# Optimization experiments

Measured on AMD Instinct MI355X. Metric: run time of the kernel, lower is better.

## Reference

```python
import jax, jax.numpy as jnp
import numpy as np

B, NQ, NK = 4, 2048, 2048
DQ = DK = DV = 256
H = 8
HD = DV // H
EPS = 1e-5


def _ln(x, g, b):
    m = jnp.mean(x, axis=-1, keepdims=True)
    v = jnp.mean(jnp.square(x - m), axis=-1, keepdims=True)
    return (x - m) * jax.lax.rsqrt(v + EPS) * g + b


def setup_inputs() -> dict:
    key = jax.random.key(0)
    ks = jax.random.split(key, 12)
    s = 0.02
    return {
        "Q": jax.random.normal(ks[0], (B, NQ, DQ), jnp.float32),
        "K": jax.random.normal(ks[1], (B, NK, DK), jnp.float32),
        "Wq": jax.random.normal(ks[2], (DV, DQ), jnp.float32) * s,
        "bq": jnp.zeros((DV,), jnp.float32),
        "Wk": jax.random.normal(ks[3], (DV, DK), jnp.float32) * s,
        "bk": jnp.zeros((DV,), jnp.float32),
        "Wv": jax.random.normal(ks[4], (DV, DK), jnp.float32) * s,
        "bv": jnp.zeros((DV,), jnp.float32),
        "Wo": jax.random.normal(ks[5], (DV, DV), jnp.float32) * s,
        "bo": jnp.zeros((DV,), jnp.float32),
        "g0": jnp.ones((DV,), jnp.float32),
        "b0": jnp.zeros((DV,), jnp.float32),
        "g1": jnp.ones((DV,), jnp.float32),
        "b1": jnp.zeros((DV,), jnp.float32),
    }


def reference(Q, K, Wq, bq, Wk, bk, Wv, bv, Wo, bo, g0, b0, g1, b1):
    Qp = Q @ Wq.T + bq            # [B,NQ,DV]
    Kp = K @ Wk.T + bk            # [B,NK,DV]
    Vp = K @ Wv.T + bv            # [B,NK,DV]
    # split(head_dim, dim=2) + cat(dim=0) == reshape heads from contiguous channel chunks
    qh = Qp.reshape(B, NQ, H, HD)
    kh = Kp.reshape(B, NK, H, HD)
    vh = Vp.reshape(B, NK, H, HD)
    scores = jnp.einsum("bqhd,bkhd->bhqk", qh, kh) / jnp.sqrt(jnp.float32(HD))
    attn = jax.nn.softmax(scores, axis=-1)          # [B,H,NQ,NK]
    o = jnp.einsum("bhqk,bkhd->bqhd", attn, vh).reshape(B, NQ, DV)
    o = _ln(o, g0, b0)
    out = o + jax.nn.relu(o @ Wo.T + bo)
    out = _ln(out, g1, b1)
    return out
```

## Files before the change

kernel.cpp:

```cpp
#include <hip/hip_runtime.h>
#include <hip/hip_bf16.h>
#include <math.h>

#define DV 256
#define NH 8
#define NB 4
#define NQ 2048
#define NKK 2048

typedef __attribute__((ext_vector_type(8))) short s8v;
typedef __attribute__((ext_vector_type(16))) float fx16;

typedef const __attribute__((address_space(1))) char g1c;
typedef __attribute__((address_space(3))) char l3c;

__device__ __forceinline__ void gl_lds16(const void* g, void* l) {
    __builtin_amdgcn_global_load_lds((g1c*)g, (l3c*)l, 16, 0, 0);
}
__device__ __forceinline__ unsigned cvtpk_bf16(float lo, float hi) {
    unsigned r;
    asm("v_cvt_pk_bf16_f32 %0, %1, %2" : "=v"(r) : "v"(lo), "v"(hi));
    return r;
}
__device__ __forceinline__ ushort f2bf(float x) {
    unsigned u = __builtin_bit_cast(unsigned, x);
    return (ushort)((u + 0x7fffu + ((u >> 16) & 1u)) >> 16);
}
__device__ __forceinline__ float bf2f(ushort h) {
    return __builtin_bit_cast(float, (unsigned)h << 16);
}

__global__ __launch_bounds__(256) void prep_w_k(
    const float* __restrict__ Wq, const float* __restrict__ Wk,
    const float* __restrict__ Wv, const float* __restrict__ Wo,
    ushort* __restrict__ Wf)
{
    const int j = blockIdx.x * 256 + threadIdx.x;
    const int w = j >> 13, c = j & 8191;
    const int bn = c >> 11, s = (c >> 8) & 7, cc = c & 255;
    const int colblk = cc >> 7, ks = (cc >> 6) & 1, g5w = (cc >> 5) & 1, l31w = cc & 31;
    const int col = bn * 64 + colblk * 32 + l31w;
    const int k = s * 32 + ks * 16 + g5w * 8;
    const float* Wsrc = (w == 0) ? Wq : (w == 1) ? Wk : (w == 2) ? Wv : Wo;
    const float* src = Wsrc + (size_t)col * 256 + k;
    float4 a = *(const float4*)src;
    float4 b = *(const float4*)(src + 4);
    uint4 pk;
    pk.x = cvtpk_bf16(a.x, a.y); pk.y = cvtpk_bf16(a.z, a.w);
    pk.z = cvtpk_bf16(b.x, b.y); pk.w = cvtpk_bf16(b.z, b.w);
    *(uint4*)(Wf + (size_t)j * 8) = pk;
}

__global__ __launch_bounds__(256) void gemm_qkv_k(
    const float* __restrict__ Qf, const float* __restrict__ Kf,
    const ushort* __restrict__ Wf,
    const float* __restrict__ bq, const float* __restrict__ bk, const float* __restrict__ bv,
    ushort* __restrict__ Qb, ushort* __restrict__ Kb, ushort* __restrict__ Vt)
{
    __shared__ __align__(16) char lds[2][20480];
    const int t = threadIdx.x, lane = t & 63, wv = t >> 6;
    const int l31 = lane & 31, g5 = lane >> 5;
    const int bm = blockIdx.x, bn = blockIdx.y;
    const int z = blockIdx.z;
    const float* Af = (z == 0) ? Qf : Kf;
    const ushort* WF = Wf + (size_t)z * 65536;
    const float* bias = (z == 0) ? bq : (z == 1) ? bk : bv;

    int arow[4], aoff[4];
#pragma unroll
    for (int k = 0; k < 4; ++k) {
        const int q = k * 256 + t, c = q >> 1, p = q & 1;
        arow[k] = bm * 128 + (c >> 7) * 32 + (c & 31);
        aoff[k] = ((c >> 6) & 1) * 16 + ((c >> 5) & 1) * 8 + p * 4;
    }
    const ushort* wsrc = WF + (size_t)(bn * 8) * 2048 + t * 8;

#pragma unroll
    for (int k = 0; k < 4; ++k)
        gl_lds16(Af + (size_t)arow[k] * 256 + aoff[k],
                 &lds[0][k * 4096 + wv * 1024 + lane * 16]);
    gl_lds16(wsrc, &lds[0][16384 + wv * 1024 + lane * 16]);
    __syncthreads();

    fx16 acc0 = {}, acc1 = {};
    for (int s = 0; s < 8; ++s) {
        const int buf = s & 1;
        if (s + 1 < 8) {
#pragma unroll
            for (int k = 0; k < 4; ++k)
                gl_lds16(Af + (size_t)arow[k] * 256 + (s + 1) * 32 + aoff[k],
                         &lds[buf ^ 1][k * 4096 + wv * 1024 + lane * 16]);
            gl_lds16(wsrc + (s + 1) * 2048, &lds[buf ^ 1][16384 + wv * 1024 + lane * 16]);
        }
        const char* Al = lds[buf];
        const char* Wl = lds[buf] + 16384;
        float4 fa0 = *(const float4*)(Al + (wv * 2 + 0) * 2048 + lane * 32);
        float4 fb0 = *(const float4*)(Al + (wv * 2 + 0) * 2048 + lane * 32 + 16);
        float4 fa1 = *(const float4*)(Al + (wv * 2 + 1) * 2048 + lane * 32);
        float4 fb1 = *(const float4*)(Al + (wv * 2 + 1) * 2048 + lane * 32 + 16);
        union { unsigned u[4]; s8v v; } A0, A1;
        A0.u[0] = cvtpk_bf16(fa0.x, fa0.y); A0.u[1] = cvtpk_bf16(fa0.z, fa0.w);
        A0.u[2] = cvtpk_bf16(fb0.x, fb0.y); A0.u[3] = cvtpk_bf16(fb0.z, fb0.w);
        A1.u[0] = cvtpk_bf16(fa1.x, fa1.y); A1.u[1] = cvtpk_bf16(fa1.z, fa1.w);
        A1.u[2] = cvtpk_bf16(fb1.x, fb1.y); A1.u[3] = cvtpk_bf16(fb1.z, fb1.w);
        s8v b00 = *(const s8v*)(Wl + 0 * 1024 + lane * 16);
        s8v b01 = *(const s8v*)(Wl + 1 * 1024 + lane * 16);
        s8v b10 = *(const s8v*)(Wl + 2 * 1024 + lane * 16);
        s8v b11 = *(const s8v*)(Wl + 3 * 1024 + lane * 16);
        __builtin_amdgcn_s_setprio(1);
        acc0 = __builtin_amdgcn_mfma_f32_32x32x16_bf16(A0.v, b00, acc0, 0, 0, 0);
        acc0 = __builtin_amdgcn_mfma_f32_32x32x16_bf16(A1.v, b01, acc0, 0, 0, 0);
        acc1 = __builtin_amdgcn_mfma_f32_32x32x16_bf16(A0.v, b10, acc1, 0, 0, 0);
        acc1 = __builtin_amdgcn_mfma_f32_32x32x16_bf16(A1.v, b11, acc1, 0, 0, 0);
        __builtin_amdgcn_s_setprio(0);
        __syncthreads();
    }

    const int row_b = bm * 128 + wv * 32;
    const float CE = 0.17677669529663687f * 1.4426950408889634f;
    const float bs0 = bias[bn * 64 + l31];
    const float bs1 = bias[bn * 64 + 32 + l31];
    if (z == 0) {
#pragma unroll
        for (int r = 0; r < 16; ++r) {
            const int row_g = row_b + (r & 3) + 8 * (r >> 2) + 4 * g5;
            Qb[(size_t)row_g * 256 + bn * 64 + l31]      = f2bf((acc0[r] + bs0) * CE);
            Qb[(size_t)row_g * 256 + bn * 64 + 32 + l31] = f2bf((acc1[r] + bs1) * CE);
        }
    } else if (z == 1) {
#pragma unroll
        for (int r = 0; r < 16; ++r) {
            const int row_g = row_b + (r & 3) + 8 * (r >> 2) + 4 * g5;
            Kb[(size_t)row_g * 256 + bn * 64 + l31]      = f2bf(acc0[r] + bs0);
            Kb[(size_t)row_g * 256 + bn * 64 + 32 + l31] = f2bf(acc1[r] + bs1);
        }
    } else {
#pragma unroll
        for (int r = 0; r < 16; ++r) {
            const int row_g = row_b + (r & 3) + 8 * (r >> 2) + 4 * g5;
            const int bb = row_g >> 11, n = row_g & 2047;
            Vt[((size_t)(bb * 8 + bn * 2 + 0) * 32 + l31) * 2048 + n] = f2bf(acc0[r] + bs0);
            Vt[((size_t)(bb * 8 + bn * 2 + 1) * 32 + l31) * 2048 + n] = f2bf(acc1[r] + bs1);
        }
    }
}

__global__ __launch_bounds__(256) void flash_mfma_k(
    const ushort* __restrict__ Qb, const ushort* __restrict__ Kb,
    const ushort* __restrict__ Vt, ushort* __restrict__ Osb, float* __restrict__ L)
{
    __shared__ __align__(16) char lds[2][8192];
    const int t = threadIdx.x;
    const int lane = t & 63, wv = t >> 6;
    const int l31 = lane & 31, g5 = lane >> 5;
    const int qt = blockIdx.x, h = blockIdx.y;
    const int b = blockIdx.z >> 1, sp = blockIdx.z & 1;

    s8v qf0, qf1;
    {
        const ushort* qp = Qb + (((size_t)b * NQ + qt * 128 + wv * 32 + l31) << 8) + h * 32 + g5 * 8;
        qf0 = *(const s8v*)(qp);
        qf1 = *(const s8v*)(qp + 16);
    }
    s8v ones;
#pragma unroll
    for (int j = 0; j < 8; ++j) ones[j] = (short)0x3F80;

    const ushort* ksrc = Kb + (((size_t)b * NKK + sp * 1024 + ((t >> 7) * 32 + (t & 31))) << 8)
                            + h * 32 + ((t >> 6) & 1) * 16 + ((t >> 5) & 1) * 8;
    const ushort* vsrc = Vt + (((size_t)(b * NH + h) * 32 + (t & 31)) << 11) + sp * 1024
                            + (t >> 6) * 16 + ((t >> 5) & 1) * 8;

    fx16 O0 = {}, lsum = {};

    gl_lds16(ksrc, &lds[0][wv * 1024]);
    gl_lds16(vsrc, &lds[0][4096 + wv * 1024]);
    __syncthreads();

    for (int kt = 0; kt < 16; ++kt) {
        const int buf = kt & 1;
        if (kt + 1 < 16) {
            gl_lds16(ksrc + (size_t)(kt + 1) * 64 * DV, &lds[buf ^ 1][wv * 1024]);
            gl_lds16(vsrc + (kt + 1) * 64, &lds[buf ^ 1][4096 + wv * 1024]);
        }
        const char* Kl = lds[buf];
        const char* Vl = lds[buf] + 4096;
        s8v kf00 = *(const s8v*)(Kl + 0 * 1024 + lane * 16);
        s8v kf01 = *(const s8v*)(Kl + 1 * 1024 + lane * 16);
        s8v kf10 = *(const s8v*)(Kl + 2 * 1024 + lane * 16);
        s8v kf11 = *(const s8v*)(Kl + 3 * 1024 + lane * 16);
        s8v vfa[4];
        vfa[0] = *(const s8v*)(Vl + 0 * 1024 + lane * 16);
        vfa[1] = *(const s8v*)(Vl + 1 * 1024 + lane * 16);
        vfa[2] = *(const s8v*)(Vl + 2 * 1024 + lane * 16);
        vfa[3] = *(const s8v*)(Vl + 3 * 1024 + lane * 16);

        fx16 z = {};
        __builtin_amdgcn_s_setprio(1);
        fx16 Sa = __builtin_amdgcn_mfma_f32_32x32x16_bf16(kf00, qf0, z, 0, 0, 0);
        Sa = __builtin_amdgcn_mfma_f32_32x32x16_bf16(kf01, qf1, Sa, 0, 0, 0);
        fx16 Sb = __builtin_amdgcn_mfma_f32_32x32x16_bf16(kf10, qf0, z, 0, 0, 0);
        Sb = __builtin_amdgcn_mfma_f32_32x32x16_bf16(kf11, qf1, Sb, 0, 0, 0);
        __builtin_amdgcn_s_setprio(0);

        float p[32];
#pragma unroll
        for (int i = 0; i < 16; ++i) {
            p[i]      = __builtin_amdgcn_exp2f(Sa[i]);
            p[16 + i] = __builtin_amdgcn_exp2f(Sb[i]);
        }

        __builtin_amdgcn_s_setprio(1);
#pragma unroll
        for (int kt2 = 0; kt2 < 4; ++kt2) {
            const int pb = 8 * kt2;
            auto ra = __builtin_amdgcn_permlane32_swap(
                cvtpk_bf16(p[pb + 0], p[pb + 1]), cvtpk_bf16(p[pb + 4], p[pb + 5]), false, false);
            auto rb = __builtin_amdgcn_permlane32_swap(
                cvtpk_bf16(p[pb + 2], p[pb + 3]), cvtpk_bf16(p[pb + 6], p[pb + 7]), false, false);
            union { unsigned u[4]; s8v v; } pf;
            pf.u[0] = ra[0]; pf.u[1] = rb[0]; pf.u[2] = ra[1]; pf.u[3] = rb[1];
            O0   = __builtin_amdgcn_mfma_f32_32x32x16_bf16(vfa[kt2], pf.v, O0, 0, 0, 0);
            lsum = __builtin_amdgcn_mfma_f32_32x32x16_bf16(ones,    pf.v, lsum, 0, 0, 0);
        }
        __builtin_amdgcn_s_setprio(0);
        __syncthreads();
    }

    {
        const int qrow = qt * 128 + wv * 32 + l31;
        ushort* dst0 = Osb + (size_t)sp * (8192 * 256)
                     + (((size_t)b * NQ + qrow) << 8) + h * 32 + g5 * 4;
#pragma unroll
        for (int rr = 0; rr < 4; ++rr) {
            uint2 w;
            w.x = cvtpk_bf16(O0[4 * rr + 0], O0[4 * rr + 1]);
            w.y = cvtpk_bf16(O0[4 * rr + 2], O0[4 * rr + 3]);
            *(uint2*)(dst0 + 8 * rr) = w;
        }
        if (g5 == 0)
            L[(((size_t)sp * NB + b) * NH + h) * NQ + qrow] = lsum[0];
    }
}

__global__ __launch_bounds__(256) void comb_ln_k(
    const ushort* __restrict__ Osb, const float* __restrict__ L,
    const float* __restrict__ g, const float* __restrict__ bb,
    ushort* __restrict__ Yb)
{
    const int t = threadIdx.x, lane = t & 63, w = t >> 6;
    const int row = blockIdx.x * 4 + w;
    const int b = row >> 11, q = row & 2047;
    const int h = lane >> 3;
    const size_t lbase = (((size_t)b * NH + h) * NQ + q);
    const size_t LS = (size_t)NB * NH * NQ;
    const float inv = 1.f / (L[lbase] + L[LS + lbase]);
    const size_t SZS = (size_t)8192 * 256;
    const size_t off = (size_t)row * 256 + lane * 4;
    const ushort4 x0 = *(const ushort4*)(Osb + off);
    const ushort4 x1 = *(const ushort4*)(Osb + SZS + off);
    float4 x;
    x.x = (bf2f(x0.x) + bf2f(x1.x)) * inv;
    x.y = (bf2f(x0.y) + bf2f(x1.y)) * inv;
    x.z = (bf2f(x0.z) + bf2f(x1.z)) * inv;
    x.w = (bf2f(x0.w) + bf2f(x1.w)) * inv;
    float s  = (x.x + x.y) + (x.z + x.w);
    float sq = fmaf(x.x, x.x, fmaf(x.y, x.y, fmaf(x.z, x.z, x.w * x.w)));
    for (int off2 = 32; off2; off2 >>= 1) {
        s  += __shfl_xor(s, off2);
        sq += __shfl_xor(sq, off2);
    }
    const float mean = s * (1.f / 256.f);
    const float var  = sq * (1.f / 256.f) - mean * mean;
    const float ri   = rsqrtf(var + 1e-5f);
    const float4 gv = *(const float4*)(g + lane * 4);
    const float4 bv = *(const float4*)(bb + lane * 4);
    uint2 p;
    p.x = cvtpk_bf16((x.x - mean) * ri * gv.x + bv.x, (x.y - mean) * ri * gv.y + bv.y);
    p.y = cvtpk_bf16((x.z - mean) * ri * gv.z + bv.z, (x.w - mean) * ri * gv.w + bv.w);
    *(uint2*)(Yb + (size_t)row * 256 + lane * 4) = p;
}

__global__ __launch_bounds__(256) void gemm_ln_k(
    const ushort* __restrict__ Ain, const ushort* __restrict__ Wfo,
    const float* __restrict__ bo, const float* __restrict__ g1,
    const float* __restrict__ b1, float* __restrict__ out)
{
    __shared__ __align__(16) char alds[32768];
    __shared__ __align__(16) char wlds[2][16384];
    __shared__ float red[4][64][2];
    __shared__ float par[64][2];
    const int t = threadIdx.x, lane = t & 63, wv = t >> 6;
    const int l31 = lane & 31, g5 = lane >> 5;
    const int row0 = blockIdx.x * 64;

#pragma unroll
    for (int it = 0; it < 8; ++it) {
        const int id = it * 256 + t;
        const int s = id >> 8, rem = id & 255, kc = rem >> 6, row = rem & 63;
        gl_lds16(Ain + (size_t)(row0 + row) * 256 + s * 32 + (kc >> 1) * 16 + (kc & 1) * 8,
                 &alds[id * 16]);
    }
#pragma unroll
    for (int it = 0; it < 4; ++it) {
        const int id = it * 256 + t;
        gl_lds16(Wfo + ((size_t)(id >> 8) * 2048 + (id & 255)) * 8, &wlds[0][id * 16]);
    }
    __syncthreads();

    fx16 acc[2][2] = {};
    for (int s = 0; s < 8; ++s) {
        const int buf = s & 1;
        if (s + 1 < 8) {
#pragma unroll
            for (int it = 0; it < 4; ++it) {
                const int id = it * 256 + t;
                gl_lds16(Wfo + ((size_t)(id >> 8) * 2048 + (s + 1) * 256 + (id & 255)) * 8,
                         &wlds[buf ^ 1][id * 16]);
            }
        }
        s8v a[2][2], bf[2][2];
#pragma unroll
        for (int rb = 0; rb < 2; ++rb)
#pragma unroll
            for (int ks = 0; ks < 2; ++ks)
                a[rb][ks] = *(const s8v*)(alds + ((s * 4 + ks * 2 + g5) * 64 + rb * 32 + l31) * 16);
#pragma unroll
        for (int ks = 0; ks < 2; ++ks)
#pragma unroll
            for (int ch = 0; ch < 2; ++ch)
                bf[ks][ch] = *(const s8v*)(wlds[buf] + (wv * 256 + ch * 128 + ks * 64 + g5 * 32 + l31) * 16);
        __builtin_amdgcn_s_setprio(1);
#pragma unroll
        for (int rb = 0; rb < 2; ++rb)
#pragma unroll
            for (int ch = 0; ch < 2; ++ch) {
                acc[rb][ch] = __builtin_amdgcn_mfma_f32_32x32x16_bf16(a[rb][0], bf[0][ch], acc[rb][ch], 0, 0, 0);
                acc[rb][ch] = __builtin_amdgcn_mfma_f32_32x32x16_bf16(a[rb][1], bf[1][ch], acc[rb][ch], 0, 0, 0);
            }
        __builtin_amdgcn_s_setprio(0);
        __syncthreads();
    }

    const int cg0 = wv * 64 + l31, cg1 = cg0 + 32;
    const float bo0 = bo[cg0], bo1 = bo[cg1];
    const int s0 = cg0 >> 5, kk0 = cg0 & 31;
    const int s1 = cg1 >> 5, kk1 = cg1 & 31;
    const int coff0 = (s0 * 4 + ((kk0 >> 4) << 1) + ((kk0 >> 3) & 1)) * 64;
    const int coff1 = (s1 * 4 + ((kk1 >> 4) << 1) + ((kk1 >> 3) & 1)) * 64;
    float x[2][2][16];
#pragma unroll
    for (int rb = 0; rb < 2; ++rb) {
#pragma unroll
        for (int r = 0; r < 16; ++r) {
            const int row = rb * 32 + (r & 3) + 8 * (r >> 2) + 4 * g5;
            const ushort h0v = *(const ushort*)(alds + ((coff0 + row) << 4) + (kk0 & 7) * 2);
            const ushort h1v = *(const ushort*)(alds + ((coff1 + row) << 4) + (kk1 & 7) * 2);
            const float x0 = bf2f(h0v) + fmaxf(acc[rb][0][r] + bo0, 0.f);
            const float x1 = bf2f(h1v) + fmaxf(acc[rb][1][r] + bo1, 0.f);
            x[rb][0][r] = x0; x[rb][1][r] = x1;
            float sv = x0 + x1;
            float sq = fmaf(x0, x0, x1 * x1);
#pragma unroll
            for (int off = 1; off < 32; off <<= 1) {
                sv += __shfl_xor(sv, off);
                sq += __shfl_xor(sq, off);
            }
            if (l31 == 0) { red[wv][row][0] = sv; red[wv][row][1] = sq; }
        }
    }
    __syncthreads();
    if (t < 64) {
        const float sv = (red[0][t][0] + red[1][t][0]) + (red[2][t][0] + red[3][t][0]);
        const float sq = (red[0][t][1] + red[1][t][1]) + (red[2][t][1] + red[3][t][1]);
        const float mean = sv * (1.f / 256.f);
        const float var  = sq * (1.f / 256.f) - mean * mean;
        par[t][0] = mean;
        par[t][1] = rsqrtf(var + 1e-5f);
    }
    __syncthreads();
    const float g1a = g1[cg0], g1b = g1[cg1];
    const float b1a = b1[cg0], b1b = b1[cg1];
#pragma unroll
    for (int rb = 0; rb < 2; ++rb) {
#pragma unroll
        for (int r = 0; r < 16; ++r) {
            const int row = rb * 32 + (r & 3) + 8 * (r >> 2) + 4 * g5;
            const float mean = par[row][0], ri = par[row][1];
            out[(size_t)(row0 + row) * 256 + cg0] = (x[rb][0][r] - mean) * ri * g1a + b1a;
            out[(size_t)(row0 + row) * 256 + cg1] = (x[rb][1][r] - mean) * ri * g1b + b1b;
        }
    }
}

extern "C" void kernel_launch(void* const* d_in, const int* in_sizes, int n_in,
                              void* d_out, int out_size, void* d_ws, size_t ws_size,
                              hipStream_t stream) {
    const float* Q  = (const float*)d_in[0];
    const float* K  = (const float*)d_in[1];
    const float* Wq = (const float*)d_in[2];
    const float* bq = (const float*)d_in[3];
    const float* Wk = (const float*)d_in[4];
    const float* bk = (const float*)d_in[5];
    const float* Wv = (const float*)d_in[6];
    const float* bv = (const float*)d_in[7];
    const float* Wo = (const float*)d_in[8];
    const float* bo = (const float*)d_in[9];
    const float* g0 = (const float*)d_in[10];
    const float* b0 = (const float*)d_in[11];
    const float* g1 = (const float*)d_in[12];
    const float* b1 = (const float*)d_in[13];
    float* out = (float*)d_out;

    char* wsb = (char*)d_ws;
    const size_t MB = 1u << 20;
    ushort* Wf  = (ushort*)(wsb + 12 * MB);
    ushort* Qb  = (ushort*)(wsb + 0 * MB);
    ushort* Kb  = (ushort*)(wsb + 4 * MB);
    ushort* Vt  = (ushort*)(wsb + 8 * MB);
    ushort* Osb = (ushort*)(wsb + 13 * MB);
    float*  L   = (float*)(wsb + 21 * MB);
    ushort* h0b = (ushort*)(wsb + 8 * MB);

    prep_w_k<<<128, 256, 0, stream>>>(Wq, Wk, Wv, Wo, Wf);
    gemm_qkv_k<<<dim3(64, 4, 3), 256, 0, stream>>>(Q, K, Wf, bq, bk, bv, Qb, Kb, Vt);
    flash_mfma_k<<<dim3(16, 8, 8), 256, 0, stream>>>(Qb, Kb, Vt, Osb, L);
    comb_ln_k<<<2048, 256, 0, stream>>>(Osb, L, g0, b0, h0b);
    gemm_ln_k<<<128, 256, 0, stream>>>(h0b, Wf + 3 * 65536, bo, g1, b1, out);
}
```

Measured before the change: 78.44 us.

## Fuse split-KV combine and first LayerNorm into output-projection GEMM kernel

Merges the combine+LayerNorm kernel into the Wo GEMM + residual + LayerNorm kernel. Each block now combines the two split partial outputs, normalizes them, and writes bf16 rows straight into LDS in the MFMA A-operand layout, so the intermediate h0 buffer never goes through global memory and one launch disappears. Block rows drop from 64 to 32, giving 256 blocks instead of 128 for better CU coverage. In exchange, each block reloads all of Wo and does half as much MFMA work per weight tile.

Result: faster. 72.33 us (-7.8%).

```diff
diff --git a/kernel.cpp b/kernel.cpp
--- a/kernel.cpp
+++ b/kernel.cpp
@@ -243,72 +243,68 @@
     }
 }
 
-__global__ __launch_bounds__(256) void comb_ln_k(
+__global__ __launch_bounds__(256) void tail_fused_k(
     const ushort* __restrict__ Osb, const float* __restrict__ L,
-    const float* __restrict__ g, const float* __restrict__ bb,
-    ushort* __restrict__ Yb)
-{
-    const int t = threadIdx.x, lane = t & 63, w = t >> 6;
-    const int row = blockIdx.x * 4 + w;
-    const int b = row >> 11, q = row & 2047;
-    const int h = lane >> 3;
-    const size_t lbase = (((size_t)b * NH + h) * NQ + q);
-    const size_t LS = (size_t)NB * NH * NQ;
-    const float inv = 1.f / (L[lbase] + L[LS + lbase]);
-    const size_t SZS = (size_t)8192 * 256;
-    const size_t off = (size_t)row * 256 + lane * 4;
-    const ushort4 x0 = *(const ushort4*)(Osb + off);
-    const ushort4 x1 = *(const ushort4*)(Osb + SZS + off);
-    float4 x;
-    x.x = (bf2f(x0.x) + bf2f(x1.x)) * inv;
-    x.y = (bf2f(x0.y) + bf2f(x1.y)) * inv;
-    x.z = (bf2f(x0.z) + bf2f(x1.z)) * inv;
-    x.w = (bf2f(x0.w) + bf2f(x1.w)) * inv;
-    float s  = (x.x + x.y) + (x.z + x.w);
-    float sq = fmaf(x.x, x.x, fmaf(x.y, x.y, fmaf(x.z, x.z, x.w * x.w)));
-    for (int off2 = 32; off2; off2 >>= 1) {
-        s  += __shfl_xor(s, off2);
-        sq += __shfl_xor(sq, off2);
-    }
-    const float mean = s * (1.f / 256.f);
-    const float var  = sq * (1.f / 256.f) - mean * mean;
-    const float ri   = rsqrtf(var + 1e-5f);
-    const float4 gv = *(const float4*)(g + lane * 4);
-    const float4 bv = *(const float4*)(bb + lane * 4);
-    uint2 p;
-    p.x = cvtpk_bf16((x.x - mean) * ri * gv.x + bv.x, (x.y - mean) * ri * gv.y + bv.y);
-    p.y = cvtpk_bf16((x.z - mean) * ri * gv.z + bv.z, (x.w - mean) * ri * gv.w + bv.w);
-    *(uint2*)(Yb + (size_t)row * 256 + lane * 4) = p;
-}
-
-__global__ __launch_bounds__(256) void gemm_ln_k(
-    const ushort* __restrict__ Ain, const ushort* __restrict__ Wfo,
+    const ushort* __restrict__ Wfo,
+    const float* __restrict__ g0, const float* __restrict__ b0,
     const float* __restrict__ bo, const float* __restrict__ g1,
     const float* __restrict__ b1, float* __restrict__ out)
 {
-    __shared__ __align__(16) char alds[32768];
+    __shared__ __align__(16) char alds[16384];
     __shared__ __align__(16) char wlds[2][16384];
-    __shared__ float red[4][64][2];
-    __shared__ float par[64][2];
+    __shared__ float red[4][32][2];
+    __shared__ float par[32][2];
     const int t = threadIdx.x, lane = t & 63, wv = t >> 6;
     const int l31 = lane & 31, g5 = lane >> 5;
-    const int row0 = blockIdx.x * 64;
-
-#pragma unroll
-    for (int it = 0; it < 8; ++it) {
-        const int id = it * 256 + t;
-        const int s = id >> 8, rem = id & 255, kc = rem >> 6, row = rem & 63;
-        gl_lds16(Ain + (size_t)(row0 + row) * 256 + s * 32 + (kc >> 1) * 16 + (kc & 1) * 8,
-                 &alds[id * 16]);
-    }
+    const int row0 = blockIdx.x * 32;
+
 #pragma unroll
     for (int it = 0; it < 4; ++it) {
         const int id = it * 256 + t;
         gl_lds16(Wfo + ((size_t)(id >> 8) * 2048 + (id & 255)) * 8, &wlds[0][id * 16]);
     }
+
+    {
+        const int h = lane >> 3;
+        const size_t SZS = (size_t)8192 * 256;
+        const size_t LS = (size_t)NB * NH * NQ;
+        const int aid0 = ((lane >> 3) * 4 + ((lane & 7) >> 1)) * 32;
+        const int abyte = (lane & 1) * 8;
+        const float4 gv = *(const float4*)(g0 + lane * 4);
+        const float4 bv = *(const float4*)(b0 + lane * 4);
+#pragma unroll
+        for (int ps = 0; ps < 8; ++ps) {
+            const int row = ps * 4 + wv;
+            const int grow = row0 + row;
+            const int b = grow >> 11, q = grow & 2047;
+            const size_t lbase = ((size_t)b * NH + h) * NQ + q;
+            const float inv = 1.f / (L[lbase] + L[LS + lbase]);
+            const size_t off = (size_t)grow * 256 + lane * 4;
+            const ushort4 x0 = *(const ushort4*)(Osb + off);
+            const ushort4 x1 = *(const ushort4*)(Osb + SZS + off);
+            float4 x;
+            x.x = (bf2f(x0.x) + bf2f(x1.x)) * inv;
+            x.y = (bf2f(x0.y) + bf2f(x1.y)) * inv;
+            x.z = (bf2f(x0.z) + bf2f(x1.z)) * inv;
+            x.w = (bf2f(x0.w) + bf2f(x1.w)) * inv;
+            float s  = (x.x + x.y) + (x.z + x.w);
+            float sq = fmaf(x.x, x.x, fmaf(x.y, x.y, fmaf(x.z, x.z, x.w * x.w)));
+            for (int o = 32; o; o >>= 1) {
+                s  += __shfl_xor(s, o);
+                sq += __shfl_xor(sq, o);
+            }
+            const float mean = s * (1.f / 256.f);
+            const float var  = sq * (1.f / 256.f) - mean * mean;
+            const float ri   = rsqrtf(var + 1e-5f);
+            uint2 p;
+            p.x = cvtpk_bf16((x.x - mean) * ri * gv.x + bv.x, (x.y - mean) * ri * gv.y + bv.y);
+            p.y = cvtpk_bf16((x.z - mean) * ri * gv.z + bv.z, (x.w - mean) * ri * gv.w + bv.w);
+            *(uint2*)(alds + (aid0 + row) * 16 + abyte) = p;
+        }
+    }
     __syncthreads();
 
-    fx16 acc[2][2] = {};
+    fx16 acc[2] = {};
     for (int s = 0; s < 8; ++s) {
         const int buf = s & 1;
         if (s + 1 < 8) {
@@ -319,12 +315,10 @@
                          &wlds[buf ^ 1][id * 16]);
             }
         }
-        s8v a[2][2], bf[2][2];
-#pragma unroll
-        for (int rb = 0; rb < 2; ++rb)
-#pragma unroll
-            for (int ks = 0; ks < 2; ++ks)
-                a[rb][ks] = *(const s8v*)(alds + ((s * 4 + ks * 2 + g5) * 64 + rb * 32 + l31) * 16);
+        s8v a[2], bf[2][2];
+#pragma unroll
+        for (int ks = 0; ks < 2; ++ks)
+            a[ks] = *(const s8v*)(alds + ((s * 4 + ks * 2 + g5) * 32 + l31) * 16);
 #pragma unroll
         for (int ks = 0; ks < 2; ++ks)
 #pragma unroll
@@ -332,12 +326,10 @@
                 bf[ks][ch] = *(const s8v*)(wlds[buf] + (wv * 256 + ch * 128 + ks * 64 + g5 * 32 + l31) * 16);
         __builtin_amdgcn_s_setprio(1);
 #pragma unroll
-        for (int rb = 0; rb < 2; ++rb)
-#pragma unroll
-            for (int ch = 0; ch < 2; ++ch) {
-                acc[rb][ch] = __builtin_amdgcn_mfma_f32_32x32x16_bf16(a[rb][0], bf[0][ch], acc[rb][ch], 0, 0, 0);
-                acc[rb][ch] = __builtin_amdgcn_mfma_f32_32x32x16_bf16(a[rb][1], bf[1][ch], acc[rb][ch], 0, 0, 0);
-            }
+        for (int ch = 0; ch < 2; ++ch) {
+            acc[ch] = __builtin_amdgcn_mfma_f32_32x32x16_bf16(a[0], bf[0][ch], acc[ch], 0, 0, 0);
+            acc[ch] = __builtin_amdgcn_mfma_f32_32x32x16_bf16(a[1], bf[1][ch], acc[ch], 0, 0, 0);
+        }
         __builtin_amdgcn_s_setprio(0);
         __syncthreads();
     }
@@ -346,31 +338,28 @@
     const float bo0 = bo[cg0], bo1 = bo[cg1];
     const int s0 = cg0 >> 5, kk0 = cg0 & 31;
     const int s1 = cg1 >> 5, kk1 = cg1 & 31;
-    const int coff0 = (s0 * 4 + ((kk0 >> 4) << 1) + ((kk0 >> 3) & 1)) * 64;
-    const int coff1 = (s1 * 4 + ((kk1 >> 4) << 1) + ((kk1 >> 3) & 1)) * 64;
-    float x[2][2][16];
-#pragma unroll
-    for (int rb = 0; rb < 2; ++rb) {
-#pragma unroll
-        for (int r = 0; r < 16; ++r) {
-            const int row = rb * 32 + (r & 3) + 8 * (r >> 2) + 4 * g5;
-            const ushort h0v = *(const ushort*)(alds + ((coff0 + row) << 4) + (kk0 & 7) * 2);
-            const ushort h1v = *(const ushort*)(alds + ((coff1 + row) << 4) + (kk1 & 7) * 2);
-            const float x0 = bf2f(h0v) + fmaxf(acc[rb][0][r] + bo0, 0.f);
-            const float x1 = bf2f(h1v) + fmaxf(acc[rb][1][r] + bo1, 0.f);
-            x[rb][0][r] = x0; x[rb][1][r] = x1;
-            float sv = x0 + x1;
-            float sq = fmaf(x0, x0, x1 * x1);
-#pragma unroll
-            for (int off = 1; off < 32; off <<= 1) {
-                sv += __shfl_xor(sv, off);
-                sq += __shfl_xor(sq, off);
-            }
-            if (l31 == 0) { red[wv][row][0] = sv; red[wv][row][1] = sq; }
-        }
+    const int coff0 = (s0 * 4 + ((kk0 >> 4) << 1) + ((kk0 >> 3) & 1)) * 32;
+    const int coff1 = (s1 * 4 + ((kk1 >> 4) << 1) + ((kk1 >> 3) & 1)) * 32;
+    float x[2][16];
+#pragma unroll
+    for (int r = 0; r < 16; ++r) {
+        const int row = (r & 3) + 8 * (r >> 2) + 4 * g5;
+        const ushort h0v = *(const ushort*)(alds + ((coff0 + row) << 4) + (kk0 & 7) * 2);
+        const ushort h1v = *(const ushort*)(alds + ((coff1 + row) << 4) + (kk1 & 7) * 2);
+        const float x0 = bf2f(h0v) + fmaxf(acc[0][r] + bo0, 0.f);
+        const float x1 = bf2f(h1v) + fmaxf(acc[1][r] + bo1, 0.f);
+        x[0][r] = x0; x[1][r] = x1;
+        float sv = x0 + x1;
+        float sq = fmaf(x0, x0, x1 * x1);
+#pragma unroll
+        for (int o = 1; o < 32; o <<= 1) {
+            sv += __shfl_xor(sv, o);
+            sq += __shfl_xor(sq, o);
+        }
+        if (l31 == 0) { red[wv][row][0] = sv; red[wv][row][1] = sq; }
     }
     __syncthreads();
-    if (t < 64) {
+    if (t < 32) {
         const float sv = (red[0][t][0] + red[1][t][0]) + (red[2][t][0] + red[3][t][0]);
         const float sq = (red[0][t][1] + red[1][t][1]) + (red[2][t][1] + red[3][t][1]);
         const float mean = sv * (1.f / 256.f);
@@ -382,14 +371,11 @@
     const float g1a = g1[cg0], g1b = g1[cg1];
     const float b1a = b1[cg0], b1b = b1[cg1];
 #pragma unroll
-    for (int rb = 0; rb < 2; ++rb) {
-#pragma unroll
-        for (int r = 0; r < 16; ++r) {
-            const int row = rb * 32 + (r & 3) + 8 * (r >> 2) + 4 * g5;
-            const float mean = par[row][0], ri = par[row][1];
-            out[(size_t)(row0 + row) * 256 + cg0] = (x[rb][0][r] - mean) * ri * g1a + b1a;
-            out[(size_t)(row0 + row) * 256 + cg1] = (x[rb][1][r] - mean) * ri * g1b + b1b;
-        }
+    for (int r = 0; r < 16; ++r) {
+        const int row = (r & 3) + 8 * (r >> 2) + 4 * g5;
+        const float mean = par[row][0], ri = par[row][1];
+        out[(size_t)(row0 + row) * 256 + cg0] = (x[0][r] - mean) * ri * g1a + b1a;
+        out[(size_t)(row0 + row) * 256 + cg1] = (x[1][r] - mean) * ri * g1b + b1b;
     }
 }
 
@@ -420,11 +406,9 @@
     ushort* Vt  = (ushort*)(wsb + 8 * MB);
     ushort* Osb = (ushort*)(wsb + 13 * MB);
     float*  L   = (float*)(wsb + 21 * MB);
-    ushort* h0b = (ushort*)(wsb + 8 * MB);
 
     prep_w_k<<<128, 256, 0, stream>>>(Wq, Wk, Wv, Wo, Wf);
     gemm_qkv_k<<<dim3(64, 4, 3), 256, 0, stream>>>(Q, K, Wf, bq, bk, bv, Qb, Kb, Vt);
     flash_mfma_k<<<dim3(16, 8, 8), 256, 0, stream>>>(Qb, Kb, Vt, Osb, L);
-    comb_ln_k<<<2048, 256, 0, stream>>>(Osb, L, g0, b0, h0b);
-    gemm_ln_k<<<128, 256, 0, stream>>>(h0b, Wf + 3 * 65536, bo, g1, b1, out);
-}
+    tail_fused_k<<<256, 256, 0, stream>>>(Osb, L, Wf + 3 * 65536, g0, b0, bo, g1, b1, out);
+}
```
